# Kernel tuning notes

Measured on AMD Instinct MI355X. Metric: run time of the kernel, lower is better.

## Reference

```python
import jax, jax.numpy as jnp
import numpy as np

N_NODES = 100000
N_EDGES = 1600000
C_IN, C_HID, C_OUT = 128, 128, 64


def setup_inputs() -> dict:
    key = jax.random.key(0)
    k1, k2, k3, k4, k5, k6 = jax.random.split(key, 6)
    x = jax.random.normal(k1, (N_NODES, C_IN), dtype=jnp.float32)
    edge_index = jax.random.randint(k2, (2, N_EDGES), 0, N_NODES, dtype=jnp.int64)
    # Glorot-style init for GCN weights, zero bias (PyG defaults)
    W1 = jax.random.normal(k3, (C_IN, C_HID), dtype=jnp.float32) * (1.0 / np.sqrt(C_IN))
    b1 = jnp.zeros((C_HID,), dtype=jnp.float32)
    W2 = jax.random.normal(k4, (C_HID, C_OUT), dtype=jnp.float32) * (1.0 / np.sqrt(C_HID))
    b2 = jnp.zeros((C_OUT,), dtype=jnp.float32)
    return {"x": x, "edge_index": edge_index, "W1": W1, "b1": b1, "W2": W2, "b2": b2}


def _gcn_conv(x, W, b, src, dst, norm, n_nodes):
    # x' = D^-1/2 (A + I) D^-1/2 (x W) + b   (PyG GCNConv default)
    h = x @ W                                  # [N, out]
    msg = h[src] * norm[:, None]               # gather + scale, [E', out]
    out = jax.ops.segment_sum(msg, dst, num_segments=n_nodes)  # scatter-add
    return out + b


def reference(x, edge_index, W1, b1, W2, b2):
    n = x.shape[0]
    loops = jnp.arange(n, dtype=edge_index.dtype)
    src = jnp.concatenate([edge_index[0], loops])  # self-loops appended
    dst = jnp.concatenate([edge_index[1], loops])
    # symmetric normalization: deg from destination index (incl. self-loops)
    deg = jax.ops.segment_sum(jnp.ones_like(dst, dtype=x.dtype), dst, num_segments=n)
    dis = jnp.where(deg > 0, jax.lax.rsqrt(deg), 0.0)
    norm = dis[src] * dis[dst]                 # [E + N]
    h = _gcn_conv(x, W1, b1, src, dst, norm, n)
    h = jax.nn.relu(h)                          # Dropout is identity at inference
    out = _gcn_conv(h, W2, b2, src, dst, norm, n)
    return out
```

## Files before the change

kernel.cpp:

```cpp
#include <hip/hip_runtime.h>

static constexpr int NPAD = 131072;
static constexpr int PAD = 48;
typedef unsigned int uint32;
typedef _Float16 f16;
typedef __attribute__((ext_vector_type(8))) _Float16 f16x8;
typedef __attribute__((ext_vector_type(4))) _Float16 f16x4;
typedef __attribute__((ext_vector_type(4))) float f32x4;

__device__ __forceinline__ ushort f2bf(float f) {
  uint32 u = __float_as_uint(f);
  return (ushort)((u + 0x7FFF + ((u >> 16) & 1)) >> 16);
}
__device__ __forceinline__ float bf_lo(uint32 u) { return __uint_as_float(u << 16); }
__device__ __forceinline__ float bf_hi(uint32 u) { return __uint_as_float(u & 0xFFFF0000u); }

__device__ __forceinline__ int lane_rank_in(unsigned long long mask) {
  return __builtin_amdgcn_mbcnt_hi((unsigned int)(mask >> 32),
                                   __builtin_amdgcn_mbcnt_lo((unsigned int)mask, 0));
}

__device__ __forceinline__ void bucket_body(const int* __restrict__ src,
                                            const int* __restrict__ dst,
                                            int* __restrict__ bcur,
                                            uint2* __restrict__ buckets,
                                            int* __restrict__ degi, int nN, int nE,
                                            unsigned long long magic, int bcap,
                                            int bb) {
  __shared__ int cnt[8];
  __shared__ int blkbase[8];
  const int t = threadIdx.x;
  {
    int z = bb * 256 + t;
    if (z < nN) degi[z] = 0;
  }
  if (t < 8) cnt[t] = 0;
  __syncthreads();
  const int e0 = bb * 2048;
  int sa[8], da[8], ba[8], off[8];
  bool va[8];
#pragma unroll
  for (int p = 0; p < 2; ++p) {
    int idx = e0 + p * 1024 + t * 4;
    if (idx + 4 <= nE) {
      int4 sv = *(const int4*)(src + idx);
      int4 dv = *(const int4*)(dst + idx);
      sa[p * 4 + 0] = sv.x; sa[p * 4 + 1] = sv.y; sa[p * 4 + 2] = sv.z; sa[p * 4 + 3] = sv.w;
      da[p * 4 + 0] = dv.x; da[p * 4 + 1] = dv.y; da[p * 4 + 2] = dv.z; da[p * 4 + 3] = dv.w;
      va[p * 4 + 0] = va[p * 4 + 1] = va[p * 4 + 2] = va[p * 4 + 3] = true;
    } else {
#pragma unroll
      for (int j = 0; j < 4; ++j) {
        int ii = idx + j;
        bool v = ii < nE;
        va[p * 4 + j] = v;
        sa[p * 4 + j] = v ? src[ii] : 0;
        da[p * 4 + j] = v ? dst[ii] : 0;
      }
    }
  }
#pragma unroll
  for (int j = 0; j < 8; ++j) {
    ba[j] = (int)(((unsigned long long)(uint32)da[j] * magic) >> 35);
    unsigned long long mv = __ballot(va[j]);
    unsigned long long m0 = __ballot((ba[j] & 1) != 0);
    unsigned long long m1 = __ballot((ba[j] & 2) != 0);
    unsigned long long m2 = __ballot((ba[j] & 4) != 0);
    unsigned long long meq = ((ba[j] & 1) ? m0 : ~m0) & ((ba[j] & 2) ? m1 : ~m1) &
                             ((ba[j] & 4) ? m2 : ~m2) & mv;
    if (va[j]) {
      int rank = lane_rank_in(meq);
      int tot = __popcll(meq);
      int leader = __ffsll(meq) - 1;
      int base = 0;
      if (rank == 0) base = atomicAdd(&cnt[ba[j]], tot);
      base = __shfl(base, leader, 64);
      off[j] = base + rank;
    } else {
      off[j] = 0;
    }
  }
  __syncthreads();
  if (t < 8) blkbase[t] = t * bcap + atomicAdd(&bcur[t], cnt[t]);
  __syncthreads();
#pragma unroll
  for (int j = 0; j < 8; ++j) {
    if (va[j]) buckets[blkbase[ba[j]] + off[j]] = make_uint2((uint32)sa[j], (uint32)da[j]);
  }
}

template <int COLS, bool RELU_IN>
__device__ __forceinline__ void gemm_mfma_body(const float* __restrict__ X,
                                               const float* __restrict__ W,
                                               ushort* __restrict__ H, int n,
                                               int bid) {
  constexpr int NS = COLS / 16;
  constexpr int LDK = 40;
  __shared__ f16 sAh[128][LDK];
  __shared__ f16 sAl[128][LDK];
  __shared__ f16 sBh[COLS][LDK];
  __shared__ f16 sBl[COLS][LDK];
  const int t = threadIdx.x;
  const int row0 = bid * 128;
  const int wv = t >> 6;
  const int l = t & 63;
  const int fr = l & 15;
  const int fkb = (l >> 4) * 8;

  f32x4 acc[2][NS];
#pragma unroll
  for (int m = 0; m < 2; ++m)
#pragma unroll
    for (int nt = 0; nt < NS; ++nt) acc[m][nt] = (f32x4){0.f, 0.f, 0.f, 0.f};

  for (int k0 = 0; k0 < 128; k0 += 32) {
#pragma unroll
    for (int p = 0; p < 4; ++p) {
      int idx = p * 256 + t;
      int r = idx >> 3;
      int f = idx & 7;
      int gr = row0 + r;
      float4 v = make_float4(0.f, 0.f, 0.f, 0.f);
      if (gr < n) v = *(const float4*)(X + (size_t)gr * 128 + k0 + f * 4);
      if (RELU_IN) {
        v.x = fmaxf(v.x, 0.f); v.y = fmaxf(v.y, 0.f);
        v.z = fmaxf(v.z, 0.f); v.w = fmaxf(v.w, 0.f);
      }
      f16x4 hv, lv;
      hv.x = (f16)v.x; lv.x = (f16)(v.x - (float)hv.x);
      hv.y = (f16)v.y; lv.y = (f16)(v.y - (float)hv.y);
      hv.z = (f16)v.z; lv.z = (f16)(v.z - (float)hv.z);
      hv.w = (f16)v.w; lv.w = (f16)(v.w - (float)hv.w);
      *(f16x4*)&sAh[r][f * 4] = hv;
      *(f16x4*)&sAl[r][f * 4] = lv;
    }
    constexpr int WP = (32 * COLS) / (256 * 4);
#pragma unroll
    for (int p = 0; p < WP; ++p) {
      int idx = p * 256 + t;
      int k = idx / (COLS / 4);
      int c4 = idx % (COLS / 4);
      float4 v = *(const float4*)(W + (size_t)(k0 + k) * COLS + c4 * 4);
      f16 hh;
      hh = (f16)v.x; sBh[c4 * 4 + 0][k] = hh; sBl[c4 * 4 + 0][k] = (f16)(v.x - (float)hh);
      hh = (f16)v.y; sBh[c4 * 4 + 1][k] = hh; sBl[c4 * 4 + 1][k] = (f16)(v.y - (float)hh);
      hh = (f16)v.z; sBh[c4 * 4 + 2][k] = hh; sBl[c4 * 4 + 2][k] = (f16)(v.z - (float)hh);
      hh = (f16)v.w; sBh[c4 * 4 + 3][k] = hh; sBl[c4 * 4 + 3][k] = (f16)(v.w - (float)hh);
    }
    __syncthreads();
    const f16x8 ah0 = *(const f16x8*)&sAh[wv * 32 + fr][fkb];
    const f16x8 ah1 = *(const f16x8*)&sAh[wv * 32 + 16 + fr][fkb];
    const f16x8 al0 = *(const f16x8*)&sAl[wv * 32 + fr][fkb];
    const f16x8 al1 = *(const f16x8*)&sAl[wv * 32 + 16 + fr][fkb];
#pragma unroll
    for (int nt = 0; nt < NS; ++nt) {
      const f16x8 bh = *(const f16x8*)&sBh[nt * 16 + fr][fkb];
      const f16x8 bl = *(const f16x8*)&sBl[nt * 16 + fr][fkb];
      acc[0][nt] = __builtin_amdgcn_mfma_f32_16x16x32_f16(ah0, bh, acc[0][nt], 0, 0, 0);
      acc[1][nt] = __builtin_amdgcn_mfma_f32_16x16x32_f16(ah1, bh, acc[1][nt], 0, 0, 0);
      acc[0][nt] = __builtin_amdgcn_mfma_f32_16x16x32_f16(al0, bh, acc[0][nt], 0, 0, 0);
      acc[1][nt] = __builtin_amdgcn_mfma_f32_16x16x32_f16(al1, bh, acc[1][nt], 0, 0, 0);
      acc[0][nt] = __builtin_amdgcn_mfma_f32_16x16x32_f16(ah0, bl, acc[0][nt], 0, 0, 0);
      acc[1][nt] = __builtin_amdgcn_mfma_f32_16x16x32_f16(ah1, bl, acc[1][nt], 0, 0, 0);
    }
    __syncthreads();
  }
#pragma unroll
  for (int m = 0; m < 2; ++m)
#pragma unroll
    for (int nt = 0; nt < NS; ++nt)
#pragma unroll
      for (int j = 0; j < 4; ++j) {
        int row = row0 + wv * 32 + m * 16 + (l >> 4) * 4 + j;
        if (row < n) H[(size_t)row * COLS + nt * 16 + fr] = f2bf(acc[m][nt][j]);
      }
}

__global__ __launch_bounds__(256) void gemm1_bucket_kernel(
    const float* __restrict__ X, const float* __restrict__ W,
    ushort* __restrict__ H, int n, const int* __restrict__ src,
    const int* __restrict__ dst, int* __restrict__ bcur,
    uint2* __restrict__ buckets, int* __restrict__ degi, int nE,
    unsigned long long magic, int bcap, int gemmBlocks) {
  const int b = (int)blockIdx.x;
  if (b < gemmBlocks) {
    gemm_mfma_body<128, false>(X, W, H, n, b);
  } else {
    bucket_body(src, dst, bcur, buckets, degi, n, nE, magic, bcap, b - gemmBlocks);
  }
}

__global__ __launch_bounds__(256) void gemm2_kernel(const float* __restrict__ X,
                                                    const float* __restrict__ W,
                                                    ushort* __restrict__ H, int n) {
  gemm_mfma_body<64, true>(X, W, H, n, (int)blockIdx.x);
}

__global__ __launch_bounds__(256) void fillpad_kernel(const uint2* __restrict__ buckets,
                                                      const int* __restrict__ bcur,
                                                      int* __restrict__ degi,
                                                      int* __restrict__ csrp, int bcap) {
  const int xcd = blockIdx.x & 7;
  const int sub = blockIdx.x >> 3;
  const int nsub = gridDim.x >> 3;
  const int cntb = bcur[xcd];
  const uint2* B = buckets + (size_t)xcd * bcap;
  for (int i = sub * 256 + threadIdx.x; i < cntb; i += nsub * 256) {
    uint2 e = B[i];
    int pos = atomicAdd(&degi[(int)e.y], 1);
    if (pos < PAD) csrp[(size_t)e.y * PAD + pos] = (int)e.x;
  }
}

template <int COLS>
__global__ __launch_bounds__(256) void agg_kernel(const int* __restrict__ degi,
                                                  const int* __restrict__ csrp,
                                                  const ushort* __restrict__ h,
                                                  const float* __restrict__ bias,
                                                  float* __restrict__ out, int n,
                                                  int nPerXcd) {
  __shared__ uint2 sE[4][64];
  const int t = threadIdx.x;
  const int lane = t & 63;
  const int wid = t >> 6;
  const int xcd = blockIdx.x & 7;
  const int sub = (int)blockIdx.x >> 3;
  const int nwv = (gridDim.x >> 3) * 4;
  const int d0 = xcd * nPerXcd;
  const int d1 = min(d0 + nPerXcd, n);
  float2 bv2 = make_float2(0.f, 0.f);
  float bv1 = 0.f;
  if (COLS == 128) bv2 = ((const float2*)bias)[lane];
  else bv1 = bias[lane];

  int d = d0 + sub * 4 + wid;
  if (d >= d1) return;

  int degA = min(degi[d], PAD);
  int sA = (lane < degA) ? csrp[(size_t)d * PAD + lane] : 0;
  float wA = (lane < degA) ? rsqrtf((float)degi[sA] + 1.0f) : 0.f;
  int dB = d + nwv;
  int degB = 0, sRawB = 0;
  if (dB < d1) {
    degB = degi[dB];
    if (lane < PAD) sRawB = csrp[(size_t)dB * PAD + lane];
  }

  while (true) {
    const float dd = rsqrtf((float)degA + 1.0f);
    const bool hasB = dB < d1;
    int sB = 0, gB = 0;
    if (hasB) {
      int dgc = min(degB, PAD);
      sB = (lane < dgc) ? sRawB : 0;
      gB = degi[sB];
    }
    const int dC = dB + nwv;
    int degC = 0, sRawC = 0;
    if (dC < d1) {
      degC = degi[dC];
      if (lane < PAD) sRawC = csrp[(size_t)dC * PAD + lane];
    }
    sE[wid][lane] = make_uint2((uint32)sA, __float_as_uint(wA));
    if (COLS == 128) {
      uint32 hv = ((const uint32*)(h + (size_t)d * 128))[lane];
      float acx = 0.f, acy = 0.f;
      for (int j0 = 0; j0 < degA; j0 += 8) {
        uint32 a[8];
        float w[8];
#pragma unroll
        for (int k = 0; k < 8; ++k) {
          uint2 e = sE[wid][j0 + k];
          w[k] = __uint_as_float(e.y);
          a[k] = ((const uint32*)(h + (size_t)e.x * 128))[lane];
        }
#pragma unroll
        for (int k = 0; k < 8; ++k) {
          acx = fmaf(w[k], bf_lo(a[k]), acx);
          acy = fmaf(w[k], bf_hi(a[k]), acy);
        }
      }
      float ox = fmaf(dd, fmaf(dd, bf_lo(hv), acx), bv2.x);
      float oy = fmaf(dd, fmaf(dd, bf_hi(hv), acy), bv2.y);
      ((float2*)(out + (size_t)d * 128))[lane] = make_float2(ox, oy);
    } else {
      uint32 hv = (uint32)h[(size_t)d * 64 + lane];
      float acc = 0.f;
      for (int j0 = 0; j0 < degA; j0 += 8) {
        uint32 a[8];
        float w[8];
#pragma unroll
        for (int k = 0; k < 8; ++k) {
          uint2 e = sE[wid][j0 + k];
          w[k] = __uint_as_float(e.y);
          a[k] = (uint32)h[(size_t)e.x * 64 + lane];
        }
#pragma unroll
        for (int k = 0; k < 8; ++k) acc = fmaf(w[k], bf_lo(a[k]), acc);
      }
      out[(size_t)d * 64 + lane] = fmaf(dd, fmaf(dd, bf_lo(hv), acc), bv1);
    }
    if (!hasB) break;
    const int dgc = min(degB, PAD);
    wA = (lane < dgc) ? rsqrtf((float)gB + 1.0f) : 0.f;
    sA = sB;
    degA = dgc;
    d = dB;
    dB = dC;
    degB = degC;
    sRawB = sRawC;
  }
}

extern "C" void kernel_launch(void* const* d_in, const int* in_sizes, int n_in,
                              void* d_out, int out_size, void* d_ws, size_t ws_size,
                              hipStream_t stream) {
  const float* x  = (const float*)d_in[0];
  const int* ei   = (const int*)d_in[1];
  const float* W1 = (const float*)d_in[2];
  const float* b1 = (const float*)d_in[3];
  const float* W2 = (const float*)d_in[4];
  const float* b2 = (const float*)d_in[5];
  float* out = (float*)d_out;

  const int N = in_sizes[0] / 128;
  const int E = in_sizes[1] / 2;
  const int* srcI = ei;
  const int* dstI = ei + E;
  const int nPerXcd = (N + 7) / 8;
  const unsigned long long magic =
      ((1ULL << 35) + (unsigned long long)nPerXcd - 1) / (unsigned long long)nPerXcd;

  char* w = (char*)d_ws;
  int* degi       = (int*)w;                   w += (size_t)NPAD * 4;
  int* bcur       = (int*)w;                   w += 64 * 4;
  int* csrp       = (int*)w;                   w += (size_t)(N + 64) * PAD * 4;
  ushort* h       = (ushort*)w;                w += (size_t)N * 128 * 2;
  float* out1     = (float*)w;
  ushort* g       = h;
  uint2* buckets  = (uint2*)out1;
  const int bcap = E / 8 + 16384;

  const int gemmBlocks = (N + 127) / 128;
  const int bucketBlocks = (E + 2047) / 2048;

  hipMemsetAsync(bcur, 0, 64 * sizeof(int), stream);
  gemm1_bucket_kernel<<<gemmBlocks + bucketBlocks, 256, 0, stream>>>(
      x, W1, h, N, srcI, dstI, bcur, buckets, degi, E, magic, bcap, gemmBlocks);
  fillpad_kernel<<<2048, 256, 0, stream>>>(buckets, bcur, degi, csrp, bcap);
  agg_kernel<128><<<2048, 256, 0, stream>>>(degi, csrp, h, b1, out1, N, nPerXcd);
  gemm2_kernel<<<gemmBlocks, 256, 0, stream>>>(out1, W2, g, N);
  agg_kernel<64><<<2048, 256, 0, stream>>>(degi, csrp, g, b2, out, N, nPerXcd);
}
```

Measured before the change: 334.6 us.

## Partition CSR fill by destination range with LDS degree counters

The CSR fill pass changes from a grid-stride loop doing global atomics on per-node degree counters to 32 blocks per XCD. Each block owns a contiguous destination-node range and keeps its degree counters in shared memory. Each block rescans its XCD's whole edge bucket with 16-byte vector loads and keeps only edges whose destination falls in its range, then writes its counters to global memory at the end. This removes about 1.7M random global atomics. In exchange, every bucket is read 32 times (mostly L2 traffic) by a smaller grid of 256 blocks.

```diff
diff --git a/kernel.cpp b/kernel.cpp
--- a/kernel.cpp
+++ b/kernel.cpp
@@ -196,20 +196,52 @@
   gemm_mfma_body<64, true>(X, W, H, n, (int)blockIdx.x);
 }
 
-__global__ __launch_bounds__(256) void fillpad_kernel(const uint2* __restrict__ buckets,
-                                                      const int* __restrict__ bcur,
-                                                      int* __restrict__ degi,
-                                                      int* __restrict__ csrp, int bcap) {
-  const int xcd = blockIdx.x & 7;
-  const int sub = blockIdx.x >> 3;
-  const int nsub = gridDim.x >> 3;
+__global__ __launch_bounds__(256) void fillpad2_kernel(
+    const uint2* __restrict__ buckets, const int* __restrict__ bcur,
+    int* __restrict__ degi, int* __restrict__ csrp, int bcap, int nPerXcd,
+    int nN, int npb) {
+  __shared__ int cnt[512];
+  const int t = threadIdx.x;
+  const int xcd = (int)blockIdx.x & 7;
+  const int sub = (int)blockIdx.x >> 3;
+  const int lo = xcd * nPerXcd + sub * npb;
+  const int hi = min(min(lo + npb, (xcd + 1) * nPerXcd), nN);
+  if (lo >= hi) return;
+  for (int k = t; k < npb; k += 256) cnt[k] = 0;
+  __syncthreads();
   const int cntb = bcur[xcd];
   const uint2* B = buckets + (size_t)xcd * bcap;
-  for (int i = sub * 256 + threadIdx.x; i < cntb; i += nsub * 256) {
-    uint2 e = B[i];
-    int pos = atomicAdd(&degi[(int)e.y], 1);
-    if (pos < PAD) csrp[(size_t)e.y * PAD + pos] = (int)e.x;
-  }
+  int i = t * 8;
+  for (; i + 7 < cntb; i += 2048) {
+    uint4 p0 = *(const uint4*)&B[i];
+    uint4 p1 = *(const uint4*)&B[i + 2];
+    uint4 p2 = *(const uint4*)&B[i + 4];
+    uint4 p3 = *(const uint4*)&B[i + 6];
+    int s[8] = {(int)p0.x, (int)p0.z, (int)p1.x, (int)p1.z,
+                (int)p2.x, (int)p2.z, (int)p3.x, (int)p3.z};
+    int d[8] = {(int)p0.y, (int)p0.w, (int)p1.y, (int)p1.w,
+                (int)p2.y, (int)p2.w, (int)p3.y, (int)p3.w};
+#pragma unroll
+    for (int k = 0; k < 8; ++k) {
+      if (d[k] >= lo && d[k] < hi) {
+        int pos = atomicAdd(&cnt[d[k] - lo], 1);
+        if (pos < PAD) csrp[(size_t)d[k] * PAD + pos] = s[k];
+      }
+    }
+  }
+  {
+    int jend = min(i + 8, cntb);
+    for (int j = i; j < jend; ++j) {
+      uint2 e = B[j];
+      int dd = (int)e.y;
+      if (dd >= lo && dd < hi) {
+        int pos = atomicAdd(&cnt[dd - lo], 1);
+        if (pos < PAD) csrp[(size_t)dd * PAD + pos] = (int)e.x;
+      }
+    }
+  }
+  __syncthreads();
+  for (int k = t; k < hi - lo; k += 256) degi[lo + k] = cnt[k];
 }
 
 template <int COLS>
@@ -343,11 +375,14 @@
 
   const int gemmBlocks = (N + 127) / 128;
   const int bucketBlocks = (E + 2047) / 2048;
+  const int SUB = 32;
+  const int npb = (nPerXcd + SUB - 1) / SUB;
 
   hipMemsetAsync(bcur, 0, 64 * sizeof(int), stream);
   gemm1_bucket_kernel<<<gemmBlocks + bucketBlocks, 256, 0, stream>>>(
       x, W1, h, N, srcI, dstI, bcur, buckets, degi, E, magic, bcap, gemmBlocks);
-  fillpad_kernel<<<2048, 256, 0, stream>>>(buckets, bcur, degi, csrp, bcap);
+  fillpad2_kernel<<<8 * SUB, 256, 0, stream>>>(buckets, bcur, degi, csrp, bcap,
+                                               nPerXcd, N, npb);
   agg_kernel<128><<<2048, 256, 0, stream>>>(degi, csrp, h, b1, out1, N, nPerXcd);
   gemm2_kernel<<<gemmBlocks, 256, 0, stream>>>(out1, W2, g, N);
   agg_kernel<64><<<2048, 256, 0, stream>>>(degi, csrp, g, b2, out, N, nPerXcd);
```

Result: slower. 354.5 us (+5.9%).
